# Kernel tuning notes

Hardware: AMD Instinct MI355X
Metric: run time of the kernel (lower is better)

Reference implementation:

```python
import jax, jax.numpy as jnp
import numpy as np

N_NODES = 100000
N_GRAPHS = 512
HID = 128
IN_DIM = 128
OUT_DIM = 10
N_EDGES = 1600000


def gcn_conv(x, src, dst, W, b, n):
    # PyG GCNConv: add self-loops, symmetric normalization D^-1/2 (A+I) D^-1/2, then linear.
    h = x @ W  # [N, H]
    deg = jnp.zeros((n,), h.dtype).at[dst].add(1.0) + 1.0  # +1 self-loop
    dinv = jax.lax.rsqrt(deg)
    norm = dinv[src] * dinv[dst]  # [E]
    agg = jnp.zeros_like(h).at[dst].add(h[src] * norm[:, None])
    agg = agg + h * (dinv * dinv)[:, None]  # self-loop messages
    return agg + b


def setup_inputs() -> dict:
    key = jax.random.key(0)
    ks = jax.random.split(key, 12)
    x = jax.random.normal(ks[0], (N_NODES, IN_DIM), jnp.float32)
    edge_index = jax.random.randint(ks[1], (2, N_EDGES), 0, N_NODES)
    batch = jnp.sort(jax.random.randint(ks[2], (N_NODES,), 0, N_GRAPHS))
    def lin(k, fan_in, shape):
        bound = 1.0 / np.sqrt(fan_in)
        return jax.random.uniform(k, shape, jnp.float32, -bound, bound)
    W1 = lin(ks[3], IN_DIM, (IN_DIM, HID)); b1 = lin(ks[4], IN_DIM, (HID,))
    W2 = lin(ks[5], HID, (HID, HID)); b2 = lin(ks[6], HID, (HID,))
    W3 = lin(ks[7], HID, (HID, HID)); b3 = lin(ks[8], HID, (HID,))
    Wc1 = lin(ks[9], 2 * HID, (2 * HID, HID)); bc1 = lin(ks[9], 2 * HID, (HID,))
    Wc2 = lin(ks[10], HID, (HID, OUT_DIM)); bc2 = lin(ks[11], HID, (OUT_DIM,))
    return {"x": x, "edge_index": edge_index, "batch": batch,
            "W1": W1, "b1": b1, "W2": W2, "b2": b2, "W3": W3, "b3": b3,
            "Wc1": Wc1, "bc1": bc1, "Wc2": Wc2, "bc2": bc2}


def reference(x, edge_index, batch, W1, b1, W2, b2, W3, b3, Wc1, bc1, Wc2, bc2):
    src, dst = edge_index[0], edge_index[1]
    n = x.shape[0]
    h = jax.nn.relu(gcn_conv(x, src, dst, W1, b1, n))
    h = jax.nn.relu(gcn_conv(h, src, dst, W2, b2, n))
    h = gcn_conv(h, src, dst, W3, b3, n)  # no relu after last conv
    # global mean pool
    sums = jax.ops.segment_sum(h, batch, num_segments=N_GRAPHS)
    cnt = jax.ops.segment_sum(jnp.ones((n,), h.dtype), batch, num_segments=N_GRAPHS)
    mean = sums / jnp.maximum(cnt, 1.0)[:, None]
    # global max pool
    mx = jax.ops.segment_max(h, batch, num_segments=N_GRAPHS)
    mx = jnp.where(jnp.isfinite(mx), mx, 0.0)
    g = jnp.concatenate([mean, mx], axis=1)  # [G, 2H]
    g = jax.nn.relu(g @ Wc1 + bc1)
    return g @ Wc2 + bc2
```

## Files before the change

### kernel.cpp

```cpp
#include <hip/hip_runtime.h>

#define H 128
#define CAP 64
#define NB 256
#define BPCAP 6144
#define EPB 8192

typedef __attribute__((ext_vector_type(8))) short bf16x8;
typedef __attribute__((ext_vector_type(4))) float f32x4;
typedef __attribute__((ext_vector_type(2))) float f32x2;

__device__ __forceinline__ unsigned short f2bf(float f) {
  unsigned u = __float_as_uint(f);
  unsigned r = u + 0x7FFFu + ((u >> 16) & 1u);
  return (unsigned short)(r >> 16);
}
__device__ __forceinline__ f32x2 up2(unsigned u) {
  return (f32x2){__uint_as_float(u << 16), __uint_as_float(u & 0xFFFF0000u)};
}

__global__ __launch_bounds__(256) void setup_all(
    const float* __restrict__ x,
    const float* __restrict__ W1, const float* __restrict__ W2, const float* __restrict__ W3,
    unsigned short* __restrict__ Xb, unsigned short* __restrict__ Wt,
    const int* __restrict__ batch, int* __restrict__ g_start, int G,
    unsigned short* __restrict__ P, unsigned short* __restrict__ Q,
    int* __restrict__ bcount,
    int n, int totalX4) {
  long long i = (long long)blockIdx.x * 256 + threadIdx.x;
  if (i < totalX4) {
    float4 v = *(const float4*)(x + i * 4);
    ushort4 o;
    o.x = f2bf(v.x); o.y = f2bf(v.y); o.z = f2bf(v.z); o.w = f2bf(v.w);
    *(ushort4*)(Xb + i * 4) = o;
    return;
  }
  i -= totalX4;
  if (i < 3 * H * H) {
    int w = (int)(i >> 14);
    int rem = (int)i & (H * H - 1);
    int c = rem >> 7;
    int k = rem & 127;
    const float* W = (w == 0) ? W1 : (w == 1) ? W2 : W3;
    Wt[i] = f2bf(W[(size_t)k * H + c]);
    return;
  }
  i -= 3 * H * H;
  if (i < n) {
    int ii = (int)i;
    int b = batch[ii];
    int prev = (ii == 0) ? -1 : batch[ii - 1];
    for (int g = prev + 1; g <= b; ++g) g_start[g] = ii;
    if (ii == n - 1) {
      for (int g = b + 1; g <= G; ++g) g_start[g] = n;
    }
    return;
  }
  i -= n;
  if (i < H) {
    P[(size_t)n * H + i] = 0;
    Q[(size_t)n * H + i] = 0;
    return;
  }
  i -= H;
  if (i < 512) bcount[i] = 0;
}

__global__ __launch_bounds__(256) void split1(
    const int* __restrict__ src, const int* __restrict__ dst,
    int2* __restrict__ buckets, int* __restrict__ bcount,
    int ne, int nbuck) {
  __shared__ int cnt[512];
  __shared__ int gbase[512];
  int tid = threadIdx.x;
  for (int i = tid; i < 512; i += 256) cnt[i] = 0;
  __syncthreads();

  int beg = blockIdx.x * EPB;
  int end = beg + EPB; if (end > ne) end = ne;

  for (int e = beg + tid; e < end; e += 256) {
    int d = dst[e];
    atomicAdd(&cnt[d >> 8], 1);
  }
  __syncthreads();
  for (int i = tid; i < nbuck; i += 256) {
    int c = cnt[i];
    gbase[i] = (c > 0) ? atomicAdd(&bcount[i], c) : 0;
    cnt[i] = 0;
  }
  __syncthreads();
  for (int e = beg + tid; e < end; e += 256) {
    int s = src[e];
    int d = dst[e];
    int b = d >> 8;
    int l = atomicAdd(&cnt[b], 1);
    int pos = gbase[b] + l;
    if (pos < BPCAP) buckets[(size_t)b * BPCAP + pos] = make_int2(s, d);
  }
}

__global__ __launch_bounds__(256) void build_csr(
    const int2* __restrict__ buckets, const int* __restrict__ bcount,
    int* __restrict__ csr_src, int* __restrict__ deg, float* __restrict__ dinv,
    int n) {
  __shared__ int cur[NB];
  int b = blockIdx.x;
  int tid = threadIdx.x;
  cur[tid] = 0;
  __syncthreads();
  int cntb = bcount[b]; if (cntb > BPCAP) cntb = BPCAP;
  const int2* bp = buckets + (size_t)b * BPCAP;
  for (int i = tid; i < cntb; i += 256) {
    int2 e = bp[i];
    int slot = atomicAdd(&cur[e.y & (NB - 1)], 1);
    if (slot < CAP) csr_src[(size_t)e.y * CAP + slot] = e.x;
  }
  __syncthreads();
  int node = b * NB + tid;
  if (node < n) {
    int d = cur[tid];
    deg[node] = d;
    dinv[node] = rsqrtf((float)(d + 1));
  }
}

#define SWLD 136
__global__ __launch_bounds__(256) void gemm_mfma(
    const unsigned short* __restrict__ Ab, const unsigned short* __restrict__ Wt,
    const float* __restrict__ dinv, unsigned short* __restrict__ outb, int n) {
  __shared__ unsigned short sW[H * SWLD];
  int tid = threadIdx.x;
  {
    int c = tid >> 1, hh = tid & 1;
    const int4* s = (const int4*)(Wt + (size_t)c * H + hh * 64);
    int4* d = (int4*)(sW + (size_t)c * SWLD + hh * 64);
#pragma unroll
    for (int i = 0; i < 8; ++i) d[i] = s[i];
  }
  __syncthreads();

  int wave = tid >> 6;
  int lane = tid & 63;
  int m = lane & 15;
  int quad = lane >> 4;
  int row = blockIdx.x * 64 + wave * 16 + m;
  bool rv = row < n;

  f32x4 acc[8];
#pragma unroll
  for (int t = 0; t < 8; ++t) acc[t] = (f32x4){0.f, 0.f, 0.f, 0.f};

  const unsigned short* arow = Ab + (size_t)(rv ? row : 0) * H;
#pragma unroll
  for (int k0 = 0; k0 < H; k0 += 32) {
    bf16x8 af;
    if (rv) af = *(const bf16x8*)(arow + k0 + quad * 8);
    else    af = (bf16x8){0, 0, 0, 0, 0, 0, 0, 0};
#pragma unroll
    for (int ct = 0; ct < 8; ++ct) {
      bf16x8 bfr = *(const bf16x8*)(sW + (size_t)(ct * 16 + m) * SWLD + k0 + quad * 8);
      acc[ct] = __builtin_amdgcn_mfma_f32_16x16x32_bf16(af, bfr, acc[ct], 0, 0, 0);
    }
  }

  __syncthreads();
  unsigned short (*sOut)[136] = (unsigned short (*)[136])sW;
  int r0 = wave * 16 + quad * 4;
#pragma unroll
  for (int r = 0; r < 4; ++r) {
    int orow = blockIdx.x * 64 + r0 + r;
    float dv = (orow < n) ? dinv[orow] : 0.f;
#pragma unroll
    for (int ct = 0; ct < 8; ++ct)
      sOut[r0 + r][ct * 16 + m] = f2bf(acc[ct][r] * dv);
  }
  __syncthreads();
  {
    int orow = blockIdx.x * 64 + (tid >> 2);
    if (orow < n) {
      const unsigned short* sp = &sOut[tid >> 2][(tid & 3) * 32];
      int4 t0 = *(const int4*)(sp + 0);
      int4 t1 = *(const int4*)(sp + 8);
      int4 t2 = *(const int4*)(sp + 16);
      int4 t3 = *(const int4*)(sp + 24);
      unsigned short* op = outb + (size_t)orow * H + (tid & 3) * 32;
      *(int4*)(op + 0)  = t0;
      *(int4*)(op + 8)  = t1;
      *(int4*)(op + 16) = t2;
      *(int4*)(op + 24) = t3;
    }
  }
}

template <bool RELU, bool OUTF32>
__global__ __launch_bounds__(256) void aggregate_bf(
    const unsigned short* __restrict__ hs, const int* __restrict__ deg_,
    const int* __restrict__ csr_src, const float* __restrict__ dinv,
    const float* __restrict__ b, void* __restrict__ outv, int n) {
  int node = blockIdx.x * 16 + (threadIdx.x >> 4);
  if (node >= n) return;
  int c = (threadIdx.x & 15) << 3;
  int deg = deg_[node]; if (deg > CAP) deg = CAP;
  int beg = node * CAP;
  int end = beg + ((deg + 7) & ~7);

  int4 sv = *(const int4*)(hs + (size_t)node * H + c);
  f32x2 a0 = up2(sv.x), a1 = up2(sv.y), a2 = up2(sv.z), a3 = up2(sv.w);

  int4 ia, ib;
  if (beg < end) {
    ia = *(const int4*)(csr_src + beg);
    ib = *(const int4*)(csr_src + beg + 4);
  }
  for (int k = beg; k < end; k += 8) {
    int4 ca = ia, cb = ib;
    int kn = k + 8;
    if (kn < end) {
      ia = *(const int4*)(csr_src + kn);
      ib = *(const int4*)(csr_src + kn + 4);
    }
    int rk = k - beg;
    if (rk + 8 > deg) {
      ca.x = (rk + 0 < deg) ? ca.x : n;
      ca.y = (rk + 1 < deg) ? ca.y : n;
      ca.z = (rk + 2 < deg) ? ca.z : n;
      ca.w = (rk + 3 < deg) ? ca.w : n;
      cb.x = (rk + 4 < deg) ? cb.x : n;
      cb.y = (rk + 5 < deg) ? cb.y : n;
      cb.z = (rk + 6 < deg) ? cb.z : n;
      cb.w = (rk + 7 < deg) ? cb.w : n;
    }
    int4 v0 = *(const int4*)(hs + (size_t)ca.x * H + c);
    int4 v1 = *(const int4*)(hs + (size_t)ca.y * H + c);
    int4 v2 = *(const int4*)(hs + (size_t)ca.z * H + c);
    int4 v3 = *(const int4*)(hs + (size_t)ca.w * H + c);
    int4 v4 = *(const int4*)(hs + (size_t)cb.x * H + c);
    int4 v5 = *(const int4*)(hs + (size_t)cb.y * H + c);
    int4 v6 = *(const int4*)(hs + (size_t)cb.z * H + c);
    int4 v7 = *(const int4*)(hs + (size_t)cb.w * H + c);
    a0 += ((up2(v0.x) + up2(v1.x)) + (up2(v2.x) + up2(v3.x))) +
          ((up2(v4.x) + up2(v5.x)) + (up2(v6.x) + up2(v7.x)));
    a1 += ((up2(v0.y) + up2(v1.y)) + (up2(v2.y) + up2(v3.y))) +
          ((up2(v4.y) + up2(v5.y)) + (up2(v6.y) + up2(v7.y)));
    a2 += ((up2(v0.z) + up2(v1.z)) + (up2(v2.z) + up2(v3.z))) +
          ((up2(v4.z) + up2(v5.z)) + (up2(v6.z) + up2(v7.z)));
    a3 += ((up2(v0.w) + up2(v1.w)) + (up2(v2.w) + up2(v3.w))) +
          ((up2(v4.w) + up2(v5.w)) + (up2(v6.w) + up2(v7.w)));
  }

  float dv = dinv[node];
  float4 b0 = *(const float4*)(b + c);
  float4 b1 = *(const float4*)(b + c + 4);
  float o0 = fmaf(a0.x, dv, b0.x), o1 = fmaf(a0.y, dv, b0.y);
  float o2 = fmaf(a1.x, dv, b0.z), o3 = fmaf(a1.y, dv, b0.w);
  float o4 = fmaf(a2.x, dv, b1.x), o5 = fmaf(a2.y, dv, b1.y);
  float o6 = fmaf(a3.x, dv, b1.z), o7 = fmaf(a3.y, dv, b1.w);
  if (RELU) {
    o0 = fmaxf(o0, 0.f); o1 = fmaxf(o1, 0.f); o2 = fmaxf(o2, 0.f); o3 = fmaxf(o3, 0.f);
    o4 = fmaxf(o4, 0.f); o5 = fmaxf(o5, 0.f); o6 = fmaxf(o6, 0.f); o7 = fmaxf(o7, 0.f);
  }
  if (OUTF32) {
    float* fo = (float*)outv + (size_t)node * H + c;
    *(float4*)(fo + 0) = make_float4(o0, o1, o2, o3);
    *(float4*)(fo + 4) = make_float4(o4, o5, o6, o7);
  } else {
    int4 ob;
    ob.x = ((unsigned)f2bf(o1) << 16) | f2bf(o0);
    ob.y = ((unsigned)f2bf(o3) << 16) | f2bf(o2);
    ob.z = ((unsigned)f2bf(o5) << 16) | f2bf(o4);
    ob.w = ((unsigned)f2bf(o7) << 16) | f2bf(o6);
    *(int4*)((unsigned short*)outv + (size_t)node * H + c) = ob;
  }
}

__global__ __launch_bounds__(256) void pool_classify(
    const float* __restrict__ h, const int* __restrict__ g_start,
    const float* __restrict__ Wc1, const float* __restrict__ bc1,
    const float* __restrict__ Wc2, const float* __restrict__ bc2,
    float* __restrict__ out) {
  __shared__ float ssum[8][128];
  __shared__ float smax[8][128];
  __shared__ float gv[2 * H];
  __shared__ float hid[H];
  int g = blockIdx.x;
  int beg = g_start[g];
  int end = g_start[g + 1];
  int q = threadIdx.x >> 5;
  int c = (threadIdx.x & 31) << 2;

  float4 s = make_float4(0.f, 0.f, 0.f, 0.f);
  float4 m = make_float4(-INFINITY, -INFINITY, -INFINITY, -INFINITY);
  for (int node = beg + q; node < end; node += 8) {
    float4 v = *(const float4*)(h + (size_t)node * H + c);
    s.x += v.x; s.y += v.y; s.z += v.z; s.w += v.w;
    m.x = fmaxf(m.x, v.x); m.y = fmaxf(m.y, v.y);
    m.z = fmaxf(m.z, v.z); m.w = fmaxf(m.w, v.w);
  }
  *(float4*)&ssum[q][c] = s;
  *(float4*)&smax[q][c] = m;
  __syncthreads();

  int cnt = end - beg;
  int t = threadIdx.x;
  if (t < 128) {
    float tot = 0.f;
#pragma unroll
    for (int qq = 0; qq < 8; ++qq) tot += ssum[qq][t];
    gv[t] = tot / fmaxf((float)cnt, 1.0f);
  } else {
    int cc = t - 128;
    float mx = -INFINITY;
#pragma unroll
    for (int qq = 0; qq < 8; ++qq) mx = fmaxf(mx, smax[qq][cc]);
    gv[H + cc] = (cnt == 0) ? 0.0f : mx;
  }
  __syncthreads();
  if (t < H) {
    float acc = 0.f;
#pragma unroll 8
    for (int k = 0; k < 2 * H; ++k) acc = fmaf(gv[k], Wc1[(size_t)k * H + t], acc);
    hid[t] = fmaxf(acc + bc1[t], 0.f);
  }
  __syncthreads();
  if (t < 10) {
    float a2 = 0.f;
    for (int j = 0; j < H; ++j) a2 = fmaf(hid[j], Wc2[(size_t)j * 10 + t], a2);
    out[(size_t)g * 10 + t] = a2 + bc2[t];
  }
}

extern "C" void kernel_launch(void* const* d_in, const int* in_sizes, int n_in,
                              void* d_out, int out_size, void* d_ws, size_t ws_size,
                              hipStream_t stream) {
  const float* x    = (const float*)d_in[0];
  const int* ei     = (const int*)d_in[1];
  const int* batch  = (const int*)d_in[2];
  const float* W1   = (const float*)d_in[3];
  const float* b1   = (const float*)d_in[4];
  const float* W2   = (const float*)d_in[5];
  const float* b2   = (const float*)d_in[6];
  const float* W3   = (const float*)d_in[7];
  const float* b3   = (const float*)d_in[8];
  const float* Wc1  = (const float*)d_in[9];
  const float* bc1  = (const float*)d_in[10];
  const float* Wc2  = (const float*)d_in[11];
  const float* bc2  = (const float*)d_in[12];
  float* out = (float*)d_out;

  const int n  = in_sizes[2];
  const int ne = in_sizes[1] / 2;
  const int G  = 512;
  const size_t NFb = (size_t)(n + 1) * H;

  const int* src = ei;
  const int* dst = ei + ne;

  unsigned short* P_bf = (unsigned short*)d_ws;
  unsigned short* Q_bf = P_bf + NFb;
  float*          F2f  = (float*)(Q_bf + NFb);
  unsigned short* Xb   = (unsigned short*)F2f;
  int* csr_src = (int*)(F2f + (size_t)n * H);
  const size_t csr_cap = (size_t)n * CAP;
  char* p = (char*)(csr_src + csr_cap);
  int*            deg      = (int*)p;            p += (size_t)n * 4;
  float*          dinv     = (float*)p;          p += (size_t)n * 4;
  int*            g_start  = (int*)p;            p += (size_t)(G + 1) * 4;
  p = (char*)(((uintptr_t)p + 255) & ~(uintptr_t)255);
  unsigned short* Wt       = (unsigned short*)p; p += (size_t)3 * H * H * 2;
  int*            bcount   = (int*)p;            p += 512 * 4;
  int2*           buckets  = (int2*)Q_bf;

  const int nbuck = (n + NB - 1) / NB;

  {
    int totalX4 = n * H / 4;
    long long tot = (long long)totalX4 + 3 * H * H + n + H + 512;
    int blocks = (int)((tot + 255) / 256);
    setup_all<<<blocks, 256, 0, stream>>>(x, W1, W2, W3, Xb, Wt,
                                          batch, g_start, G,
                                          P_bf, Q_bf, bcount, n, totalX4);
  }

  split1<<<(ne + EPB - 1) / EPB, 256, 0, stream>>>(src, dst, buckets, bcount, ne, nbuck);
  build_csr<<<nbuck, 256, 0, stream>>>(buckets, bcount, csr_src, deg, dinv, n);

  const int tile_grid = (n + 63) / 64;
  const int node_grid = (n + 15) / 16;

  gemm_mfma<<<tile_grid, 256, 0, stream>>>(Xb, Wt, dinv, Q_bf, n);
  aggregate_bf<true, false><<<node_grid, 256, 0, stream>>>(Q_bf, deg, csr_src, dinv, b1, P_bf, n);

  gemm_mfma<<<tile_grid, 256, 0, stream>>>(P_bf, Wt + H * H, dinv, Q_bf, n);
  aggregate_bf<true, false><<<node_grid, 256, 0, stream>>>(Q_bf, deg, csr_src, dinv, b2, P_bf, n);

  gemm_mfma<<<tile_grid, 256, 0, stream>>>(P_bf, Wt + 2 * H * H, dinv, Q_bf, n);
  aggregate_bf<false, true><<<node_grid, 256, 0, stream>>>(Q_bf, deg, csr_src, dinv, b3, F2f, n);

  pool_classify<<<G, 256, 0, stream>>>(F2f, g_start, Wc1, bc1, Wc2, bc2, out);
}
```

Baseline: 439.3 us.

## Fuse neighbor aggregation with MFMA transform by reordering to aggregate-then-multiply

Each GCN layer is reordered from A(XW) to (AX)W. A single kernel now gathers the neighbor rows of 64 nodes into LDS, then multiplies that tile by W with MFMA and applies bias, ReLU and the next layer's dinv prescale in the epilogue. The first layer's dinv scaling moves into the input bf16 conversion, so CSR construction now runs before setup, and the bucket counter is cleared with a memset. This removes three kernel launches and one full-size intermediate write and read per layer. In exchange W is read from global memory instead of LDS, and each thread gathers four nodes one after another, which may hide gather latency less well.

```diff
diff --git a/kernel.cpp b/kernel.cpp
--- a/kernel.cpp
+++ b/kernel.cpp
@@ -5,6 +5,7 @@
 #define NB 256
 #define BPCAP 6144
 #define EPB 8192
+#define SWLD 136
 
 typedef __attribute__((ext_vector_type(8))) short bf16x8;
 typedef __attribute__((ext_vector_type(4))) float f32x4;
@@ -20,19 +21,20 @@
 }
 
 __global__ __launch_bounds__(256) void setup_all(
-    const float* __restrict__ x,
+    const float* __restrict__ x, const float* __restrict__ dinv,
     const float* __restrict__ W1, const float* __restrict__ W2, const float* __restrict__ W3,
-    unsigned short* __restrict__ Xb, unsigned short* __restrict__ Wt,
+    unsigned short* __restrict__ T0, unsigned short* __restrict__ Wt,
     const int* __restrict__ batch, int* __restrict__ g_start, int G,
     unsigned short* __restrict__ P, unsigned short* __restrict__ Q,
-    int* __restrict__ bcount,
     int n, int totalX4) {
   long long i = (long long)blockIdx.x * 256 + threadIdx.x;
   if (i < totalX4) {
+    float dv = dinv[(int)(i >> 5)];
     float4 v = *(const float4*)(x + i * 4);
     ushort4 o;
-    o.x = f2bf(v.x); o.y = f2bf(v.y); o.z = f2bf(v.z); o.w = f2bf(v.w);
-    *(ushort4*)(Xb + i * 4) = o;
+    o.x = f2bf(v.x * dv); o.y = f2bf(v.y * dv);
+    o.z = f2bf(v.z * dv); o.w = f2bf(v.w * dv);
+    *(ushort4*)(T0 + i * 4) = o;
     return;
   }
   i -= totalX4;
@@ -58,12 +60,10 @@
   }
   i -= n;
   if (i < H) {
+    T0[(size_t)n * H + i] = 0;
     P[(size_t)n * H + i] = 0;
     Q[(size_t)n * H + i] = 0;
-    return;
-  }
-  i -= H;
-  if (i < 512) bcount[i] = 0;
+  }
 }
 
 __global__ __launch_bounds__(256) void split1(
@@ -125,18 +125,81 @@
   }
 }
 
-#define SWLD 136
-__global__ __launch_bounds__(256) void gemm_mfma(
-    const unsigned short* __restrict__ Ab, const unsigned short* __restrict__ Wt,
-    const float* __restrict__ dinv, unsigned short* __restrict__ outb, int n) {
-  __shared__ unsigned short sW[H * SWLD];
+template <bool MID>
+__global__ __launch_bounds__(256) void agg_gemm(
+    const unsigned short* __restrict__ T, const int* __restrict__ deg_,
+    const int* __restrict__ csr_src, const float* __restrict__ dinv,
+    const unsigned short* __restrict__ Wt, const float* __restrict__ bias,
+    void* __restrict__ outv, int n) {
+  __shared__ unsigned short sA[64 * SWLD];
   int tid = threadIdx.x;
+  int blk = blockIdx.x;
+
   {
-    int c = tid >> 1, hh = tid & 1;
-    const int4* s = (const int4*)(Wt + (size_t)c * H + hh * 64);
-    int4* d = (int4*)(sW + (size_t)c * SWLD + hh * 64);
-#pragma unroll
-    for (int i = 0; i < 8; ++i) d[i] = s[i];
+    int l16 = tid & 15;
+    int grp = tid >> 4;
+    int c = l16 << 3;
+    for (int iter = 0; iter < 4; ++iter) {
+      int lrow = iter * 16 + grp;
+      int node = blk * 64 + lrow;
+      int nd = (node < n) ? node : n;
+      int deg = (node < n) ? deg_[node] : 0;
+      if (deg > CAP) deg = CAP;
+      int beg = nd * CAP;
+      int end = beg + ((deg + 7) & ~7);
+
+      int4 sv = *(const int4*)(T + (size_t)nd * H + c);
+      f32x2 a0 = up2(sv.x), a1 = up2(sv.y), a2 = up2(sv.z), a3 = up2(sv.w);
+
+      int4 ia, ib;
+      if (beg < end) {
+        ia = *(const int4*)(csr_src + beg);
+        ib = *(const int4*)(csr_src + beg + 4);
+      }
+      for (int k = beg; k < end; k += 8) {
+        int4 ca = ia, cb = ib;
+        int kn = k + 8;
+        if (kn < end) {
+          ia = *(const int4*)(csr_src + kn);
+          ib = *(const int4*)(csr_src + kn + 4);
+        }
+        int rk = k - beg;
+        if (rk + 8 > deg) {
+          ca.x = (rk + 0 < deg) ? ca.x : n;
+          ca.y = (rk + 1 < deg) ? ca.y : n;
+          ca.z = (rk + 2 < deg) ? ca.z : n;
+          ca.w = (rk + 3 < deg) ? ca.w : n;
+          cb.x = (rk + 4 < deg) ? cb.x : n;
+          cb.y = (rk + 5 < deg) ? cb.y : n;
+          cb.z = (rk + 6 < deg) ? cb.z : n;
+          cb.w = (rk + 7 < deg) ? cb.w : n;
+        }
+        int4 v0 = *(const int4*)(T + (size_t)ca.x * H + c);
+        int4 v1 = *(const int4*)(T + (size_t)ca.y * H + c);
+        int4 v2 = *(const int4*)(T + (size_t)ca.z * H + c);
+        int4 v3 = *(const int4*)(T + (size_t)ca.w * H + c);
+        int4 v4 = *(const int4*)(T + (size_t)cb.x * H + c);
+        int4 v5 = *(const int4*)(T + (size_t)cb.y * H + c);
+        int4 v6 = *(const int4*)(T + (size_t)cb.z * H + c);
+        int4 v7 = *(const int4*)(T + (size_t)cb.w * H + c);
+        a0 += ((up2(v0.x) + up2(v1.x)) + (up2(v2.x) + up2(v3.x))) +
+              ((up2(v4.x) + up2(v5.x)) + (up2(v6.x) + up2(v7.x)));
+        a1 += ((up2(v0.y) + up2(v1.y)) + (up2(v2.y) + up2(v3.y))) +
+              ((up2(v4.y) + up2(v5.y)) + (up2(v6.y) + up2(v7.y)));
+        a2 += ((up2(v0.z) + up2(v1.z)) + (up2(v2.z) + up2(v3.z))) +
+              ((up2(v4.z) + up2(v5.z)) + (up2(v6.z) + up2(v7.z)));
+        a3 += ((up2(v0.w) + up2(v1.w)) + (up2(v2.w) + up2(v3.w))) +
+              ((up2(v4.w) + up2(v5.w)) + (up2(v6.w) + up2(v7.w)));
+      }
+
+      float dv = (node < n) ? dinv[node] : 0.f;
+      int4 ob;
+      ob.x = ((unsigned)f2bf(a0.y * dv) << 16) | f2bf(a0.x * dv);
+      ob.y = ((unsigned)f2bf(a1.y * dv) << 16) | f2bf(a1.x * dv);
+      ob.z = ((unsigned)f2bf(a2.y * dv) << 16) | f2bf(a2.x * dv);
+      ob.w = ((unsigned)f2bf(a3.y * dv) << 16) | f2bf(a3.x * dv);
+      *(int4*)(sA + (size_t)lrow * SWLD + c) = ob;
+    }
   }
   __syncthreads();
 
@@ -144,133 +207,63 @@
   int lane = tid & 63;
   int m = lane & 15;
   int quad = lane >> 4;
-  int row = blockIdx.x * 64 + wave * 16 + m;
-  bool rv = row < n;
 
   f32x4 acc[8];
 #pragma unroll
   for (int t = 0; t < 8; ++t) acc[t] = (f32x4){0.f, 0.f, 0.f, 0.f};
 
-  const unsigned short* arow = Ab + (size_t)(rv ? row : 0) * H;
+  const unsigned short* aw = sA + (size_t)(wave * 16 + m) * SWLD;
 #pragma unroll
   for (int k0 = 0; k0 < H; k0 += 32) {
-    bf16x8 af;
-    if (rv) af = *(const bf16x8*)(arow + k0 + quad * 8);
-    else    af = (bf16x8){0, 0, 0, 0, 0, 0, 0, 0};
+    bf16x8 af = *(const bf16x8*)(aw + k0 + quad * 8);
 #pragma unroll
     for (int ct = 0; ct < 8; ++ct) {
-      bf16x8 bfr = *(const bf16x8*)(sW + (size_t)(ct * 16 + m) * SWLD + k0 + quad * 8);
+      bf16x8 bfr = *(const bf16x8*)(Wt + (size_t)(ct * 16 + m) * H + k0 + quad * 8);
       acc[ct] = __builtin_amdgcn_mfma_f32_16x16x32_bf16(af, bfr, acc[ct], 0, 0, 0);
     }
   }
 
-  __syncthreads();
-  unsigned short (*sOut)[136] = (unsigned short (*)[136])sW;
+  float bv[8];
+#pragma unroll
+  for (int ct = 0; ct < 8; ++ct) bv[ct] = bias[ct * 16 + m];
   int r0 = wave * 16 + quad * 4;
-#pragma unroll
-  for (int r = 0; r < 4; ++r) {
-    int orow = blockIdx.x * 64 + r0 + r;
-    float dv = (orow < n) ? dinv[orow] : 0.f;
-#pragma unroll
-    for (int ct = 0; ct < 8; ++ct)
-      sOut[r0 + r][ct * 16 + m] = f2bf(acc[ct][r] * dv);
-  }
-  __syncthreads();
-  {
-    int orow = blockIdx.x * 64 + (tid >> 2);
+
+  if (MID) {
+    __syncthreads();
+#pragma unroll
+    for (int r = 0; r < 4; ++r) {
+      int orow = blk * 64 + r0 + r;
+      float dv = (orow < n) ? dinv[orow] : 0.f;
+#pragma unroll
+      for (int ct = 0; ct < 8; ++ct)
+        sA[(size_t)(r0 + r) * SWLD + ct * 16 + m] =
+            f2bf(fmaxf(acc[ct][r] + bv[ct], 0.f) * dv);
+    }
+    __syncthreads();
+    int orow = blk * 64 + (tid >> 2);
     if (orow < n) {
-      const unsigned short* sp = &sOut[tid >> 2][(tid & 3) * 32];
+      const unsigned short* sp = sA + (size_t)(tid >> 2) * SWLD + (tid & 3) * 32;
       int4 t0 = *(const int4*)(sp + 0);
       int4 t1 = *(const int4*)(sp + 8);
       int4 t2 = *(const int4*)(sp + 16);
       int4 t3 = *(const int4*)(sp + 24);
-      unsigned short* op = outb + (size_t)orow * H + (tid & 3) * 32;
+      unsigned short* op = (unsigned short*)outv + (size_t)orow * H + (tid & 3) * 32;
       *(int4*)(op + 0)  = t0;
       *(int4*)(op + 8)  = t1;
       *(int4*)(op + 16) = t2;
       *(int4*)(op + 24) = t3;
     }
-  }
-}
-
-template <bool RELU, bool OUTF32>
-__global__ __launch_bounds__(256) void aggregate_bf(
-    const unsigned short* __restrict__ hs, const int* __restrict__ deg_,
-    const int* __restrict__ csr_src, const float* __restrict__ dinv,
-    const float* __restrict__ b, void* __restrict__ outv, int n) {
-  int node = blockIdx.x * 16 + (threadIdx.x >> 4);
-  if (node >= n) return;
-  int c = (threadIdx.x & 15) << 3;
-  int deg = deg_[node]; if (deg > CAP) deg = CAP;
-  int beg = node * CAP;
-  int end = beg + ((deg + 7) & ~7);
-
-  int4 sv = *(const int4*)(hs + (size_t)node * H + c);
-  f32x2 a0 = up2(sv.x), a1 = up2(sv.y), a2 = up2(sv.z), a3 = up2(sv.w);
-
-  int4 ia, ib;
-  if (beg < end) {
-    ia = *(const int4*)(csr_src + beg);
-    ib = *(const int4*)(csr_src + beg + 4);
-  }
-  for (int k = beg; k < end; k += 8) {
-    int4 ca = ia, cb = ib;
-    int kn = k + 8;
-    if (kn < end) {
-      ia = *(const int4*)(csr_src + kn);
-      ib = *(const int4*)(csr_src + kn + 4);
-    }
-    int rk = k - beg;
-    if (rk + 8 > deg) {
-      ca.x = (rk + 0 < deg) ? ca.x : n;
-      ca.y = (rk + 1 < deg) ? ca.y : n;
-      ca.z = (rk + 2 < deg) ? ca.z : n;
-      ca.w = (rk + 3 < deg) ? ca.w : n;
-      cb.x = (rk + 4 < deg) ? cb.x : n;
-      cb.y = (rk + 5 < deg) ? cb.y : n;
-      cb.z = (rk + 6 < deg) ? cb.z : n;
-      cb.w = (rk + 7 < deg) ? cb.w : n;
-    }
-    int4 v0 = *(const int4*)(hs + (size_t)ca.x * H + c);
-    int4 v1 = *(const int4*)(hs + (size_t)ca.y * H + c);
-    int4 v2 = *(const int4*)(hs + (size_t)ca.z * H + c);
-    int4 v3 = *(const int4*)(hs + (size_t)ca.w * H + c);
-    int4 v4 = *(const int4*)(hs + (size_t)cb.x * H + c);
-    int4 v5 = *(const int4*)(hs + (size_t)cb.y * H + c);
-    int4 v6 = *(const int4*)(hs + (size_t)cb.z * H + c);
-    int4 v7 = *(const int4*)(hs + (size_t)cb.w * H + c);
-    a0 += ((up2(v0.x) + up2(v1.x)) + (up2(v2.x) + up2(v3.x))) +
-          ((up2(v4.x) + up2(v5.x)) + (up2(v6.x) + up2(v7.x)));
-    a1 += ((up2(v0.y) + up2(v1.y)) + (up2(v2.y) + up2(v3.y))) +
-          ((up2(v4.y) + up2(v5.y)) + (up2(v6.y) + up2(v7.y)));
-    a2 += ((up2(v0.z) + up2(v1.z)) + (up2(v2.z) + up2(v3.z))) +
-          ((up2(v4.z) + up2(v5.z)) + (up2(v6.z) + up2(v7.z)));
-    a3 += ((up2(v0.w) + up2(v1.w)) + (up2(v2.w) + up2(v3.w))) +
-          ((up2(v4.w) + up2(v5.w)) + (up2(v6.w) + up2(v7.w)));
-  }
-
-  float dv = dinv[node];
-  float4 b0 = *(const float4*)(b + c);
-  float4 b1 = *(const float4*)(b + c + 4);
-  float o0 = fmaf(a0.x, dv, b0.x), o1 = fmaf(a0.y, dv, b0.y);
-  float o2 = fmaf(a1.x, dv, b0.z), o3 = fmaf(a1.y, dv, b0.w);
-  float o4 = fmaf(a2.x, dv, b1.x), o5 = fmaf(a2.y, dv, b1.y);
-  float o6 = fmaf(a3.x, dv, b1.z), o7 = fmaf(a3.y, dv, b1.w);
-  if (RELU) {
-    o0 = fmaxf(o0, 0.f); o1 = fmaxf(o1, 0.f); o2 = fmaxf(o2, 0.f); o3 = fmaxf(o3, 0.f);
-    o4 = fmaxf(o4, 0.f); o5 = fmaxf(o5, 0.f); o6 = fmaxf(o6, 0.f); o7 = fmaxf(o7, 0.f);
-  }
-  if (OUTF32) {
-    float* fo = (float*)outv + (size_t)node * H + c;
-    *(float4*)(fo + 0) = make_float4(o0, o1, o2, o3);
-    *(float4*)(fo + 4) = make_float4(o4, o5, o6, o7);
   } else {
-    int4 ob;
-    ob.x = ((unsigned)f2bf(o1) << 16) | f2bf(o0);
-    ob.y = ((unsigned)f2bf(o3) << 16) | f2bf(o2);
-    ob.z = ((unsigned)f2bf(o5) << 16) | f2bf(o4);
-    ob.w = ((unsigned)f2bf(o7) << 16) | f2bf(o6);
-    *(int4*)((unsigned short*)outv + (size_t)node * H + c) = ob;
+    float* fo = (float*)outv;
+#pragma unroll
+    for (int r = 0; r < 4; ++r) {
+      int orow = blk * 64 + r0 + r;
+      if (orow < n) {
+#pragma unroll
+        for (int ct = 0; ct < 8; ++ct)
+          fo[(size_t)orow * H + ct * 16 + m] = acc[ct][r] + bv[ct];
+      }
+    }
   }
 }
 
@@ -359,7 +352,7 @@
   unsigned short* P_bf = (unsigned short*)d_ws;
   unsigned short* Q_bf = P_bf + NFb;
   float*          F2f  = (float*)(Q_bf + NFb);
-  unsigned short* Xb   = (unsigned short*)F2f;
+  unsigned short* T0   = (unsigned short*)F2f;
   int* csr_src = (int*)(F2f + (size_t)n * H);
   const size_t csr_cap = (size_t)n * CAP;
   char* p = (char*)(csr_src + csr_cap);
@@ -373,29 +366,23 @@
 
   const int nbuck = (n + NB - 1) / NB;
 
+  hipMemsetAsync(bcount, 0, 512 * sizeof(int), stream);
+  split1<<<(ne + EPB - 1) / EPB, 256, 0, stream>>>(src, dst, buckets, bcount, ne, nbuck);
+  build_csr<<<nbuck, 256, 0, stream>>>(buckets, bcount, csr_src, deg, dinv, n);
+
   {
     int totalX4 = n * H / 4;
-    long long tot = (long long)totalX4 + 3 * H * H + n + H + 512;
+    long long tot = (long long)totalX4 + 3 * H * H + n + H;
     int blocks = (int)((tot + 255) / 256);
-    setup_all<<<blocks, 256, 0, stream>>>(x, W1, W2, W3, Xb, Wt,
-                                          batch, g_start, G,
-                                          P_bf, Q_bf, bcount, n, totalX4);
-  }
-
-  split1<<<(ne + EPB - 1) / EPB, 256, 0, stream>>>(src, dst, buckets, bcount, ne, nbuck);
-  build_csr<<<nbuck, 256, 0, stream>>>(buckets, bcount, csr_src, deg, dinv, n);
+    setup_all<<<blocks, 256, 0, stream>>>(x, dinv, W1, W2, W3, T0, Wt,
+                                          batch, g_start, G, P_bf, Q_bf, n, totalX4);
+  }
 
   const int tile_grid = (n + 63) / 64;
-  const int node_grid = (n + 15) / 16;
-
-  gemm_mfma<<<tile_grid, 256, 0, stream>>>(Xb, Wt, dinv, Q_bf, n);
-  aggregate_bf<true, false><<<node_grid, 256, 0, stream>>>(Q_bf, deg, csr_src, dinv, b1, P_bf, n);
-
-  gemm_mfma<<<tile_grid, 256, 0, stream>>>(P_bf, Wt + H * H, dinv, Q_bf, n);
-  aggregate_bf<true, false><<<node_grid, 256, 0, stream>>>(Q_bf, deg, csr_src, dinv, b2, P_bf, n);
-
-  gemm_mfma<<<tile_grid, 256, 0, stream>>>(P_bf, Wt + 2 * H * H, dinv, Q_bf, n);
-  aggregate_bf<false, true><<<node_grid, 256, 0, stream>>>(Q_bf, deg, csr_src, dinv, b3, F2f, n);
+
+  agg_gemm<true><<<tile_grid, 256, 0, stream>>>(T0, deg, csr_src, dinv, Wt, b1, P_bf, n);
+  agg_gemm<true><<<tile_grid, 256, 0, stream>>>(P_bf, deg, csr_src, dinv, Wt + H * H, b2, Q_bf, n);
+  agg_gemm<false><<<tile_grid, 256, 0, stream>>>(Q_bf, deg, csr_src, dinv, Wt + 2 * H * H, b3, F2f, n);
 
   pool_classify<<<G, 256, 0, stream>>>(F2f, g_start, Wc1, bc1, Wc2, bc2, out);
 }
```

New measurement: 445.9 us. Within noise of the previous version (+1.5%).
